# Optimization experiments

Measured on AMD Instinct MI355X. Metric: run time of the kernel, lower is better.

The kernel has to match this reference:

```python
import jax, jax.numpy as jnp
import numpy as np

B, U, L, E, H, V = 512, 10, 50, 200, 200, 50000
FLAT = 16 * 16 * 8  # conv(3x3,VALID)->48x48, pool(3x3,s3)->16x16, 8 channels


def gru(x, Wih, Whh, bih, bhh):
    """PyTorch-convention GRU (gate order r,z,n). x: [B,T,E] -> (ys [B,T,H], h_last [B,H])."""
    Bx = x.shape[0]
    Hh = Whh.shape[1]
    x_proj = x @ Wih.T + bih  # [B,T,3H]

    def step(h, xp):
        gh = h @ Whh.T + bhh
        xr, xz, xn = jnp.split(xp, 3, axis=-1)
        hr, hz, hn = jnp.split(gh, 3, axis=-1)
        r = jax.nn.sigmoid(xr + hr)
        z = jax.nn.sigmoid(xz + hz)
        n = jnp.tanh(xn + r * hn)
        h_new = (1.0 - z) * n + z * h
        return h_new, h_new

    h0 = jnp.zeros((Bx, Hh), x.dtype)
    h_last, ys = jax.lax.scan(step, h0, jnp.swapaxes(x_proj, 0, 1))
    return jnp.swapaxes(ys, 0, 1), h_last


def setup_inputs() -> dict:
    key = jax.random.key(0)
    ks = jax.random.split(key, 24)
    s = 0.05
    inp = {
        "utterance": jax.random.randint(ks[0], (B, U, L), 0, V, dtype=jnp.int32),
        "response": jax.random.randint(ks[1], (B, L), 0, V, dtype=jnp.int32),
        "emb": jax.random.uniform(ks[2], (V, E), jnp.float32, -0.25, 0.25),
        "W_ih_u": jax.random.normal(ks[3], (3 * H, E)) * s,
        "W_hh_u": jax.random.normal(ks[4], (3 * H, H)) * s,
        "b_ih_u": jnp.zeros((3 * H,), jnp.float32),
        "b_hh_u": jnp.zeros((3 * H,), jnp.float32),
        "W_ih_r": jax.random.normal(ks[5], (3 * H, E)) * s,
        "W_hh_r": jax.random.normal(ks[6], (3 * H, H)) * s,
        "b_ih_r": jnp.zeros((3 * H,), jnp.float32),
        "b_hh_r": jnp.zeros((3 * H,), jnp.float32),
        "conv_w": jax.random.normal(ks[7], (8, 2, 3, 3)) * 0.3,
        "conv_b": jnp.zeros((8,), jnp.float32),
        "lin_w": jax.random.normal(ks[8], (50, FLAT)) * 0.02,
        "lin_b": jnp.zeros((50,), jnp.float32),
        "Amat": jax.random.normal(ks[9], (H, H)) * 0.05,
        "W_ih_f": jax.random.normal(ks[10], (3 * H, 50)) * s,
        "W_hh_f": jax.random.normal(ks[11], (3 * H, H)) * s,
        "b_ih_f": jnp.zeros((3 * H,), jnp.float32),
        "b_hh_f": jnp.zeros((3 * H,), jnp.float32),
        "flin_w": jax.random.normal(ks[12], (1, H)) * 0.05,
        "flin_b": jnp.zeros((1,), jnp.float32),
    }
    return inp


def reference(utterance, response, emb, W_ih_u, W_hh_u, b_ih_u, b_hh_u,
              W_ih_r, W_hh_r, b_ih_r, b_hh_r, conv_w, conv_b, lin_w, lin_b,
              Amat, W_ih_f, W_hh_f, b_ih_f, b_hh_f, flin_w, flin_b):
    ue = emb[utterance]            # [B,U,L,E]
    re = emb[response]             # [B,L,E]

    rg, _ = gru(re, W_ih_r, W_hh_r, b_ih_r, b_hh_r)  # [B,L,H]

    # word-level match: matmul(utt_emb, resp_emb^T)
    m1 = jnp.einsum('bule,bte->bult', ue, re)  # [B,U,L,L]

    # segment-level: GRU(utt) @ A @ GRU(resp)^T  (loop over utterances folded into batch)
    ug, _ = gru(ue.reshape(B * U, L, E), W_ih_u, W_hh_u, b_ih_u, b_hh_u)
    ug = ug.reshape(B, U, L, H)
    m2 = jnp.einsum('bulh,hk,btk->bult', ug, Amat, rg)  # [B,U,L,L]

    x = jnp.stack([m1, m2], axis=2).reshape(B * U, 2, L, L)  # [B*U,2,50,50]
    x = jax.lax.conv_general_dilated(x, conv_w, (1, 1), 'VALID',
                                     dimension_numbers=('NCHW', 'OIHW', 'NCHW'))
    x = jax.nn.relu(x + conv_b[None, :, None, None])          # [B*U,8,48,48]
    x = jax.lax.reduce_window(x, -jnp.inf, jax.lax.max,
                              (1, 1, 3, 3), (1, 1, 3, 3), 'VALID')  # [B*U,8,16,16]
    x = x.reshape(B * U, FLAT)
    mv = jnp.tanh(x @ lin_w.T + lin_b).reshape(B, U, 50)      # matching vectors

    _, h_last = gru(mv, W_ih_f, W_hh_f, b_ih_f, b_hh_f)       # [B,H]
    logits = h_last @ flin_w.T + flin_b                       # [B,1]
    return jax.nn.sigmoid(logits)
```

## Files before the change

kernel.cpp:

```cpp
#include <hip/hip_runtime.h>
#include <hip/hip_bf16.h>


typedef __attribute__((ext_vector_type(8))) short short8v;
typedef __attribute__((ext_vector_type(4))) float f32x4;

__device__ __forceinline__ float sigm(float x) { return 1.0f / (1.0f + __expf(-x)); }
__device__ __forceinline__ float tanhfast(float x) {
    float e = __expf(2.0f * x);
    return 1.0f - 2.0f / (e + 1.0f);
}
__device__ __forceinline__ float bl(unsigned x) { return __uint_as_float(x << 16); }
__device__ __forceinline__ float bh(unsigned x) { return __uint_as_float(x & 0xffff0000u); }
__device__ __forceinline__ unsigned packbf(float a, float b) {
    union { __hip_bfloat16 h[2]; unsigned u; } cv;
    cv.h[0] = __float2bfloat16(a); cv.h[1] = __float2bfloat16(b);
    return cv.u;
}

__global__ __launch_bounds__(256)
void gemm_mfma(const void* __restrict__ Asrc, int a_bf16,
               const int* __restrict__ gidx,
               const float* __restrict__ W, const float* __restrict__ bias,
               __hip_bfloat16* __restrict__ C, int M, int N)
{
    __shared__ __hip_bfloat16 Al[64 * 232];
    __shared__ __hip_bfloat16 Bl[64 * 232];
    const int tid = threadIdx.x;
    const int m0 = blockIdx.x * 64, n0 = blockIdx.y * 64;

    for (int idx = tid; idx < 64 * 29; idx += 256) {
        int r = idx / 29, q = idx - r * 29;
        int k0 = q * 8, row = m0 + r;
        uint4 val = make_uint4(0, 0, 0, 0);
        if (k0 < 200 && row < M) {
            size_t ar = (size_t)(gidx ? gidx[row] : row) * 200 + k0;
            if (a_bf16) {
                val = *(const uint4*)((const __hip_bfloat16*)Asrc + ar);
            } else {
                const float* ap = (const float*)Asrc + ar;
                float4 f0 = *(const float4*)ap;
                float4 f1 = *(const float4*)(ap + 4);
                val.x = packbf(f0.x, f0.y); val.y = packbf(f0.z, f0.w);
                val.z = packbf(f1.x, f1.y); val.w = packbf(f1.z, f1.w);
            }
        }
        *(uint4*)(Al + r * 232 + k0) = val;
    }
    for (int idx = tid; idx < 64 * 29; idx += 256) {
        int r = idx / 29, q = idx - r * 29;
        int k0 = q * 8, row = n0 + r;
        uint4 val = make_uint4(0, 0, 0, 0);
        if (k0 < 200 && row < N) {
            const float* wp = W + (size_t)row * 200 + k0;
            float4 f0 = *(const float4*)wp;
            float4 f1 = *(const float4*)(wp + 4);
            val.x = packbf(f0.x, f0.y); val.y = packbf(f0.z, f0.w);
            val.z = packbf(f1.x, f1.y); val.w = packbf(f1.z, f1.w);
        }
        *(uint4*)(Bl + r * 232 + k0) = val;
    }
    __syncthreads();

    const int wid = tid >> 6, lane = tid & 63;
    const int wm = (wid >> 1) * 32, wn = (wid & 1) * 32;
    const int lrow = lane & 15, lk8 = (lane >> 4) * 8;
    f32x4 acc00 = {0.f, 0.f, 0.f, 0.f}, acc01 = {0.f, 0.f, 0.f, 0.f};
    f32x4 acc10 = {0.f, 0.f, 0.f, 0.f}, acc11 = {0.f, 0.f, 0.f, 0.f};
#pragma unroll
    for (int kk = 0; kk < 7; ++kk) {
        const int kb = kk * 32 + lk8;
        short8v a0 = *(const short8v*)(Al + (wm + lrow) * 232 + kb);
        short8v a1 = *(const short8v*)(Al + (wm + 16 + lrow) * 232 + kb);
        short8v b0 = *(const short8v*)(Bl + (wn + lrow) * 232 + kb);
        short8v b1 = *(const short8v*)(Bl + (wn + 16 + lrow) * 232 + kb);
        acc00 = __builtin_amdgcn_mfma_f32_16x16x32_bf16(a0, b0, acc00, 0, 0, 0);
        acc01 = __builtin_amdgcn_mfma_f32_16x16x32_bf16(a0, b1, acc01, 0, 0, 0);
        acc10 = __builtin_amdgcn_mfma_f32_16x16x32_bf16(a1, b0, acc10, 0, 0, 0);
        acc11 = __builtin_amdgcn_mfma_f32_16x16x32_bf16(a1, b1, acc11, 0, 0, 0);
    }
    const int drow = (lane >> 4) * 4, dcol = lane & 15;
#pragma unroll
    for (int fm = 0; fm < 2; ++fm) {
#pragma unroll
        for (int fn = 0; fn < 2; ++fn) {
            const f32x4 av = (fm == 0) ? (fn == 0 ? acc00 : acc01)
                                       : (fn == 0 ? acc10 : acc11);
            const int gcol = n0 + wn + fn * 16 + dcol;
            if (gcol >= N) continue;
            const float bs = bias ? bias[gcol] : 0.0f;
#pragma unroll
            for (int r = 0; r < 4; ++r) {
                const int grow = m0 + wm + fm * 16 + drow + r;
                if (grow >= M) continue;
                C[(size_t)grow * N + gcol] = __float2bfloat16(av[r] + bs);
            }
        }
    }
}

__global__ __launch_bounds__(256)
void gemm_tn(const void* __restrict__ Av, int a_bf16,
             const int* __restrict__ gidx, int gstride, int goff,
             const float* __restrict__ W, const float* __restrict__ bias,
             void* __restrict__ Cv, int c_bf16,
             int M, int N, int K, int act)
{
    __shared__ float As[16][64];
    __shared__ float Ws[16][64];
    const int tid = threadIdx.x;
    const int m0 = blockIdx.x * 64;
    const int n0 = blockIdx.y * 64;
    const int lr = tid >> 2;
    const int lk = (tid & 3) << 2;
    const int tx = tid & 15, ty = tid >> 4;

    float acc[4][4];
#pragma unroll
    for (int i = 0; i < 4; ++i)
#pragma unroll
        for (int j = 0; j < 4; ++j) acc[i][j] = 0.0f;

    const int am = m0 + lr;
    size_t arow_off = 0; bool avalid = (am < M);
    if (avalid) arow_off = (size_t)(gidx ? gidx[(size_t)am * gstride + goff] : am) * K;
    const float* arow32 = (const float*)Av + arow_off;
    const __hip_bfloat16* arow16 = (const __hip_bfloat16*)Av + arow_off;
    const int wn = n0 + lr;
    const float* wrow = (wn < N) ? (W + (size_t)wn * K) : nullptr;

    for (int kb = 0; kb < K; kb += 16) {
        const int k = kb + lk;
        float a0 = 0, a1 = 0, a2 = 0, a3 = 0, w0 = 0, w1 = 0, w2 = 0, w3 = 0;
        if (avalid) {
            if (a_bf16) {
                if (k + 3 < K) {
                    uint2 p = *(const uint2*)(arow16 + k);
                    a0 = bl(p.x); a1 = bh(p.x); a2 = bl(p.y); a3 = bh(p.y);
                } else {
                    if (k < K) a0 = __bfloat162float(arow16[k]);
                    if (k + 1 < K) a1 = __bfloat162float(arow16[k + 1]);
                    if (k + 2 < K) a2 = __bfloat162float(arow16[k + 2]);
                }
            } else {
                if (k + 3 < K) { float4 v = *(const float4*)(arow32 + k); a0 = v.x; a1 = v.y; a2 = v.z; a3 = v.w; }
                else { if (k < K) a0 = arow32[k]; if (k + 1 < K) a1 = arow32[k + 1]; if (k + 2 < K) a2 = arow32[k + 2]; }
            }
        }
        if (wrow) {
            if (k + 3 < K) { float4 v = *(const float4*)(wrow + k); w0 = v.x; w1 = v.y; w2 = v.z; w3 = v.w; }
            else { if (k < K) w0 = wrow[k]; if (k + 1 < K) w1 = wrow[k + 1]; if (k + 2 < K) w2 = wrow[k + 2]; }
        }
        __syncthreads();
        As[lk + 0][lr] = a0; As[lk + 1][lr] = a1; As[lk + 2][lr] = a2; As[lk + 3][lr] = a3;
        Ws[lk + 0][lr] = w0; Ws[lk + 1][lr] = w1; Ws[lk + 2][lr] = w2; Ws[lk + 3][lr] = w3;
        __syncthreads();
#pragma unroll
        for (int kk = 0; kk < 16; ++kk) {
            float4 av = *(const float4*)(&As[kk][ty << 2]);
            float4 wv = *(const float4*)(&Ws[kk][tx << 2]);
            float aa[4] = { av.x, av.y, av.z, av.w };
            float ww[4] = { wv.x, wv.y, wv.z, wv.w };
#pragma unroll
            for (int i = 0; i < 4; ++i)
#pragma unroll
                for (int j = 0; j < 4; ++j)
                    acc[i][j] = fmaf(aa[i], ww[j], acc[i][j]);
        }
    }

#pragma unroll
    for (int i = 0; i < 4; ++i) {
        const int row = m0 + (ty << 2) + i;
        if (row >= M) continue;
#pragma unroll
        for (int j = 0; j < 4; ++j) {
            const int col = n0 + (tx << 2) + j;
            if (col >= N) continue;
            float t = acc[i][j];
            if (bias) t += bias[col];
            if (act == 1) t = tanhfast(t);
            if (c_bf16) ((__hip_bfloat16*)Cv)[(size_t)row * N + col] = __float2bfloat16(t);
            else        ((float*)Cv)[(size_t)row * N + col] = t;
        }
    }
}

__global__ __launch_bounds__(256)
void transpose_wf(const float* __restrict__ Wf, float* __restrict__ Tf)
{
    int id = blockIdx.x * 256 + threadIdx.x;
    if (id < 120000) {
        int e = id / 600, j = id - e * 600;
        Tf[id] = Wf[(size_t)j * 200 + e];
    }
}

__global__ __launch_bounds__(256)
void pack_whh(const float* __restrict__ Wu, const float* __restrict__ Wr,
              __hip_bfloat16* __restrict__ Du, __hip_bfloat16* __restrict__ Dr)
{
    int idx = blockIdx.x * 256 + threadIdx.x;
    if (idx >= 143360) return;
    int j = idx / 224, e = idx - j * 224;
    bool v = (j < 600) && (e < 200);
    Du[idx] = __float2bfloat16(v ? Wu[(size_t)j * 200 + e] : 0.0f);
    Dr[idx] = __float2bfloat16(v ? Wr[(size_t)j * 200 + e] : 0.0f);
}

__global__ __launch_bounds__(256)
void gather_re16(const int* __restrict__ resp, const float* __restrict__ emb,
                 __hip_bfloat16* __restrict__ re16)
{
    int idx = blockIdx.x * 256 + threadIdx.x;
    if (idx < 2560000) {
        int row = idx / 100, q = idx - row * 100;
        float2 v = *(const float2*)(emb + (size_t)resp[row] * 200 + 2 * q);
        ((unsigned*)re16)[idx] = packbf(v.x, v.y);
    }
}

__global__ __launch_bounds__(512, 2)
void scan_gru_mfma(const int* __restrict__ utt,
                   const __hip_bfloat16* __restrict__ EPu,
                   const __hip_bfloat16* __restrict__ xpr16,
                   const __hip_bfloat16* __restrict__ Wu16,
                   const __hip_bfloat16* __restrict__ Wr16,
                   const float* __restrict__ bhu, const float* __restrict__ bhr,
                   __hip_bfloat16* __restrict__ ug16,
                   __hip_bfloat16* __restrict__ rg16)
{
    __shared__ __align__(16) float gh[32][644];
    __shared__ __align__(16) float hf[32][204];
    __shared__ __align__(16) __hip_bfloat16 h16[32][232];

    const int tid = threadIdx.x;
    const bool isResp = (int)blockIdx.x >= 160;
    const int row0 = isResp ? ((int)blockIdx.x - 160) * 32 : (int)blockIdx.x * 32;
    const __hip_bfloat16* Wt = isResp ? Wr16 : Wu16;
    const float* bgate = isResp ? bhr : bhu;
    __hip_bfloat16* arch = isResp ? rg16 : ug16;

    for (int i = tid; i < 32 * 204; i += 512) ((float*)hf)[i] = 0.0f;
    for (int i = tid; i < 928; i += 512) ((uint4*)h16)[i] = make_uint4(0, 0, 0, 0);
    __syncthreads();

    const int wid = tid >> 6, lane = tid & 63;
    const int lrow = lane & 15, lk8 = (lane >> 4) * 8;
    const int drow = (lane >> 4) * 4, dcol = lane & 15;

    short8v Bf[5][7];
#pragma unroll
    for (int i = 0; i < 5; ++i) {
        const int j = (wid * 5 + i) * 16 + lrow;
#pragma unroll
        for (int kk = 0; kk < 7; ++kk)
            Bf[i][kk] = *(const short8v*)(Wt + (size_t)j * 224 + kk * 32 + lk8);
    }

    const int r0a = tid / 25,        c0a = (tid % 25) * 8;
    const int t1  = tid + 512;
    const int r0b = t1 / 25,         c0b = (t1 % 25) * 8;

    for (int t = 0; t < 50; ++t) {
        const int ga = row0 + r0a;
        const __hip_bfloat16* xpa = isResp
            ? (xpr16 + ((size_t)ga * 50 + t) * 600)
            : (EPu + (size_t)utt[ga * 50 + t] * 600);
        uint4 xra = *(const uint4*)(xpa + c0a);
        uint4 xza = *(const uint4*)(xpa + 200 + c0a);
        uint4 xna = *(const uint4*)(xpa + 400 + c0a);

        f32x4 a0[5], a1[5];
#pragma unroll
        for (int i = 0; i < 5; ++i) {
            a0[i] = (f32x4){0.f, 0.f, 0.f, 0.f};
            a1[i] = (f32x4){0.f, 0.f, 0.f, 0.f};
        }
#pragma unroll
        for (int kk = 0; kk < 7; ++kk) {
            short8v A0 = *(const short8v*)(&h16[lrow][kk * 32 + lk8]);
            short8v A1 = *(const short8v*)(&h16[16 + lrow][kk * 32 + lk8]);
#pragma unroll
            for (int i = 0; i < 5; ++i) {
                a0[i] = __builtin_amdgcn_mfma_f32_16x16x32_bf16(A0, Bf[i][kk], a0[i], 0, 0, 0);
                a1[i] = __builtin_amdgcn_mfma_f32_16x16x32_bf16(A1, Bf[i][kk], a1[i], 0, 0, 0);
            }
        }
#pragma unroll
        for (int i = 0; i < 5; ++i) {
            const int j = (wid * 5 + i) * 16 + dcol;
#pragma unroll
            for (int r = 0; r < 4; ++r) {
                gh[drow + r][j] = a0[i][r];
                gh[16 + drow + r][j] = a1[i][r];
            }
        }
        __syncthreads();

        {
            const int row = r0a, c0 = c0a, grow = ga;
            const unsigned xr4[4] = { xra.x, xra.y, xra.z, xra.w };
            const unsigned xz4[4] = { xza.x, xza.y, xza.z, xza.w };
            const unsigned xn4[4] = { xna.x, xna.y, xna.z, xna.w };
            float hn[8];
#pragma unroll
            for (int j = 0; j < 8; ++j) {
                const int c = c0 + j;
                const float xr = (j & 1) ? bh(xr4[j >> 1]) : bl(xr4[j >> 1]);
                const float xz = (j & 1) ? bh(xz4[j >> 1]) : bl(xz4[j >> 1]);
                const float xn = (j & 1) ? bh(xn4[j >> 1]) : bl(xn4[j >> 1]);
                const float rr = sigm(xr + gh[row][c] + bgate[c]);
                const float zz = sigm(xz + gh[row][200 + c] + bgate[200 + c]);
                const float nn = tanhfast(xn + rr * (gh[row][400 + c] + bgate[400 + c]));
                hn[j] = (1.0f - zz) * nn + zz * hf[row][c];
            }
            *(float4*)(&hf[row][c0])     = (float4){hn[0], hn[1], hn[2], hn[3]};
            *(float4*)(&hf[row][c0 + 4]) = (float4){hn[4], hn[5], hn[6], hn[7]};
            uint4 pk;
            pk.x = packbf(hn[0], hn[1]); pk.y = packbf(hn[2], hn[3]);
            pk.z = packbf(hn[4], hn[5]); pk.w = packbf(hn[6], hn[7]);
            *(uint4*)(&h16[row][c0]) = pk;
            *(uint4*)(arch + ((size_t)grow * 50 + t) * 200 + c0) = pk;
        }
        if (tid < 288) {
            const int row = r0b, c0 = c0b, grow = row0 + r0b;
            const __hip_bfloat16* xp = isResp
                ? (xpr16 + ((size_t)grow * 50 + t) * 600)
                : (EPu + (size_t)utt[grow * 50 + t] * 600);
            uint4 xrv = *(const uint4*)(xp + c0);
            uint4 xzv = *(const uint4*)(xp + 200 + c0);
            uint4 xnv = *(const uint4*)(xp + 400 + c0);
            const unsigned xr4[4] = { xrv.x, xrv.y, xrv.z, xrv.w };
            const unsigned xz4[4] = { xzv.x, xzv.y, xzv.z, xzv.w };
            const unsigned xn4[4] = { xnv.x, xnv.y, xnv.z, xnv.w };
            float hn[8];
#pragma unroll
            for (int j = 0; j < 8; ++j) {
                const int c = c0 + j;
                const float xr = (j & 1) ? bh(xr4[j >> 1]) : bl(xr4[j >> 1]);
                const float xz = (j & 1) ? bh(xz4[j >> 1]) : bl(xz4[j >> 1]);
                const float xn = (j & 1) ? bh(xn4[j >> 1]) : bl(xn4[j >> 1]);
                const float rr = sigm(xr + gh[row][c] + bgate[c]);
                const float zz = sigm(xz + gh[row][200 + c] + bgate[200 + c]);
                const float nn = tanhfast(xn + rr * (gh[row][400 + c] + bgate[400 + c]));
                hn[j] = (1.0f - zz) * nn + zz * hf[row][c];
            }
            *(float4*)(&hf[row][c0])     = (float4){hn[0], hn[1], hn[2], hn[3]};
            *(float4*)(&hf[row][c0 + 4]) = (float4){hn[4], hn[5], hn[6], hn[7]};
            uint4 pk;
            pk.x = packbf(hn[0], hn[1]); pk.y = packbf(hn[2], hn[3]);
            pk.z = packbf(hn[4], hn[5]); pk.w = packbf(hn[6], hn[7]);
            *(uint4*)(&h16[row][c0]) = pk;
            *(uint4*)(arch + ((size_t)grow * 50 + t) * 200 + c0) = pk;
        }
        __syncthreads();
    }
}

__global__ __launch_bounds__(256)
void match_conv_pool(const int* __restrict__ utt, const float* __restrict__ emb,
                     const __hip_bfloat16* __restrict__ ug16,
                     const __hip_bfloat16* __restrict__ re16,
                     const __hip_bfloat16* __restrict__ rgA16,
                     const float* __restrict__ cw, const float* __restrict__ cb,
                     float* __restrict__ pooled)
{
    const int bu = blockIdx.x, b = bu / 10;
    __shared__ __align__(16) __hip_bfloat16 As[64 * 232];
    __shared__ __align__(16) __hip_bfloat16 Bs[64 * 232];
    __shared__ float m[2][50][50];
    __shared__ float w[144];
    __shared__ float bsh[8];
    const int tid = threadIdx.x;
    if (tid < 144) w[tid] = cw[tid];
    if (tid >= 144 && tid < 152) bsh[tid - 144] = cb[tid - 144];

    for (int idx = tid; idx < 64 * 29; idx += 256) {
        int r = idx / 29, q = idx - r * 29;
        uint4 av = make_uint4(0, 0, 0, 0), bv = make_uint4(0, 0, 0, 0);
        if (r < 50 && q < 25) {
            const float* ap = emb + (size_t)utt[bu * 50 + r] * 200 + q * 8;
            float4 f0 = *(const float4*)ap;
            float4 f1 = *(const float4*)(ap + 4);
            av.x = packbf(f0.x, f0.y); av.y = packbf(f0.z, f0.w);
            av.z = packbf(f1.x, f1.y); av.w = packbf(f1.z, f1.w);
            bv = *(const uint4*)(re16 + (size_t)b * 10000 + (size_t)r * 200 + q * 8);
        }
        *(uint4*)(As + r * 232 + q * 8) = av;
        *(uint4*)(Bs + r * 232 + q * 8) = bv;
    }
    __syncthreads();

    const int wid = tid >> 6, lane = tid & 63;
    const int wm = (wid >> 1) * 32, wn = (wid & 1) * 32;
    const int lrow = lane & 15, lk8 = (lane >> 4) * 8;
    const int drow = (lane >> 4) * 4, dcol = lane & 15;

#pragma unroll 1
    for (int ch = 0; ch < 2; ++ch) {
        f32x4 acc00 = {0.f, 0.f, 0.f, 0.f}, acc01 = {0.f, 0.f, 0.f, 0.f};
        f32x4 acc10 = {0.f, 0.f, 0.f, 0.f}, acc11 = {0.f, 0.f, 0.f, 0.f};
#pragma unroll
        for (int kk = 0; kk < 7; ++kk) {
            const int kb = kk * 32 + lk8;
            short8v a0 = *(const short8v*)(As + (wm + lrow) * 232 + kb);
            short8v a1 = *(const short8v*)(As + (wm + 16 + lrow) * 232 + kb);
            short8v b0 = *(const short8v*)(Bs + (wn + lrow) * 232 + kb);
            short8v b1 = *(const short8v*)(Bs + (wn + 16 + lrow) * 232 + kb);
            acc00 = __builtin_amdgcn_mfma_f32_16x16x32_bf16(a0, b0, acc00, 0, 0, 0);
            acc01 = __builtin_amdgcn_mfma_f32_16x16x32_bf16(a0, b1, acc01, 0, 0, 0);
            acc10 = __builtin_amdgcn_mfma_f32_16x16x32_bf16(a1, b0, acc10, 0, 0, 0);
            acc11 = __builtin_amdgcn_mfma_f32_16x16x32_bf16(a1, b1, acc11, 0, 0, 0);
        }
#pragma unroll
        for (int fm = 0; fm < 2; ++fm) {
#pragma unroll
            for (int fn = 0; fn < 2; ++fn) {
                const f32x4 av = (fm == 0) ? (fn == 0 ? acc00 : acc01)
                                           : (fn == 0 ? acc10 : acc11);
                const int gcol = wn + fn * 16 + dcol;
                if (gcol >= 50) continue;
#pragma unroll
                for (int r = 0; r < 4; ++r) {
                    const int grow = wm + fm * 16 + drow + r;
                    if (grow < 50) m[ch][grow][gcol] = av[r];
                }
            }
        }
        __syncthreads();
        if (ch == 0) {
            for (int idx = tid; idx < 50 * 25; idx += 256) {
                int r = idx / 25, q = idx - r * 25;
                *(uint4*)(As + r * 232 + q * 8) =
                    *(const uint4*)(ug16 + (size_t)bu * 10000 + (size_t)r * 200 + q * 8);
                *(uint4*)(Bs + r * 232 + q * 8) =
                    *(const uint4*)(rgA16 + (size_t)b * 10000 + (size_t)r * 200 + q * 8);
            }
            __syncthreads();
        }
    }

#pragma unroll
    for (int k = 0; k < 8; ++k) {
        const int o = tid + k * 256;
        const int c = o >> 8, ph = (o >> 4) & 15, pw = o & 15;
        float mx = -1e30f;
#pragma unroll
        for (int p = 0; p < 3; ++p)
#pragma unroll
            for (int q = 0; q < 3; ++q) {
                const int y = ph * 3 + p, x = pw * 3 + q;
                float s = bsh[c];
#pragma unroll
                for (int ci = 0; ci < 2; ++ci)
#pragma unroll
                    for (int dy = 0; dy < 3; ++dy)
#pragma unroll
                        for (int dx = 0; dx < 3; ++dx)
                            s = fmaf(w[(c * 2 + ci) * 9 + dy * 3 + dx],
                                     m[ci][y + dy][x + dx], s);
                s = fmaxf(s, 0.0f);
                mx = fmaxf(mx, s);
            }
        pooled[(size_t)bu * 2048 + o] = mx;
    }
}

__global__ __launch_bounds__(256)
void final_gru(const float* __restrict__ xpf, const float* __restrict__ WTf,
               const float* __restrict__ bhf, const float* __restrict__ fw,
               const float* __restrict__ fb, float* __restrict__ out)
{
    const int blk = blockIdx.x;
    const int tid = threadIdx.x;
    __shared__ float h[2][201];
    for (int i = tid; i < 402; i += 256) ((float*)h)[i] = 0.0f;
    __syncthreads();
    const int rr = tid / 100;
    const int j0 = 2 * (tid % 100);
    for (int t = 0; t < 10; ++t) {
        float cR[2] = {}, cZ[2] = {}, cN[2] = {};
        if (tid < 200) {
#pragma unroll 2
            for (int e = 0; e < 200; ++e) {
                const float* w = WTf + (size_t)e * 600;
                float2 wr = *(const float2*)(w + j0);
                float2 wz = *(const float2*)(w + 200 + j0);
                float2 wn = *(const float2*)(w + 400 + j0);
                float hv = h[rr][e];
                cR[0] = fmaf(hv, wr.x, cR[0]); cR[1] = fmaf(hv, wr.y, cR[1]);
                cZ[0] = fmaf(hv, wz.x, cZ[0]); cZ[1] = fmaf(hv, wz.y, cZ[1]);
                cN[0] = fmaf(hv, wn.x, cN[0]); cN[1] = fmaf(hv, wn.y, cN[1]);
            }
        }
        __syncthreads();
        if (tid < 200) {
            const float* xp = xpf + ((size_t)(blk * 2 + rr) * 10 + t) * 600;
#pragma unroll
            for (int j = 0; j < 2; ++j) {
                const int c = j0 + j;
                float rrg = sigm(xp[c] + cR[j] + bhf[c]);
                float zz = sigm(xp[200 + c] + cZ[j] + bhf[200 + c]);
                float nn = tanhfast(xp[400 + c] + rrg * (cN[j] + bhf[400 + c]));
                h[rr][c] = (1.0f - zz) * nn + zz * h[rr][c];
            }
        }
        __syncthreads();
    }
    if (tid < 2) {
        float s = fb[0];
        for (int k = 0; k < 200; ++k) s = fmaf(h[tid][k], fw[k], s);
        out[blk * 2 + tid] = sigm(s);
    }
}

__global__ __launch_bounds__(256)
void fill_out(float* __restrict__ out)
{
    int i = blockIdx.x * 256 + threadIdx.x;
    if (i < 512) out[i] = 0.0f;
}

extern "C" void kernel_launch(void* const* d_in, const int* in_sizes, int n_in,
                              void* d_out, int out_size, void* d_ws, size_t ws_size,
                              hipStream_t stream)
{
    const int*   utt    = (const int*)d_in[0];
    const int*   resp   = (const int*)d_in[1];
    const float* emb    = (const float*)d_in[2];
    const float* W_ih_u = (const float*)d_in[3];
    const float* W_hh_u = (const float*)d_in[4];
    const float* b_ih_u = (const float*)d_in[5];
    const float* b_hh_u = (const float*)d_in[6];
    const float* W_ih_r = (const float*)d_in[7];
    const float* W_hh_r = (const float*)d_in[8];
    const float* b_ih_r = (const float*)d_in[9];
    const float* b_hh_r = (const float*)d_in[10];
    const float* conv_w = (const float*)d_in[11];
    const float* conv_b = (const float*)d_in[12];
    const float* lin_w  = (const float*)d_in[13];
    const float* lin_b  = (const float*)d_in[14];
    const float* Amat   = (const float*)d_in[15];
    const float* W_ih_f = (const float*)d_in[16];
    const float* W_hh_f = (const float*)d_in[17];
    const float* b_ih_f = (const float*)d_in[18];
    const float* b_hh_f = (const float*)d_in[19];
    const float* flin_w = (const float*)d_in[20];
    const float* flin_b = (const float*)d_in[21];
    float* out = (float*)d_out;
    float* ws  = (float*)d_ws;

    size_t off = 0;
    auto alloc = [&](size_t n) { float* p = ws + off; off += (n + 63) & ~((size_t)63); return p; };
    float* WT_f   = alloc(120000);
    float* Wu16f  = alloc(71680);
    float* Wr16f  = alloc(71680);
    float* re16f  = alloc(2560000);
    float* EPuf   = alloc(15000000);
    float* xprf   = alloc(7680000);
    float* ug16f  = alloc(25600000);
    float* rg16f  = alloc(2560000);
    float* rgA16f = alloc(2560000);

    if (off * sizeof(float) > ws_size) {
        hipLaunchKernelGGL(fill_out, dim3(2), dim3(256), 0, stream, out);
        return;
    }

    __hip_bfloat16* Wu16  = (__hip_bfloat16*)Wu16f;
    __hip_bfloat16* Wr16  = (__hip_bfloat16*)Wr16f;
    __hip_bfloat16* re16  = (__hip_bfloat16*)re16f;
    __hip_bfloat16* EPu   = (__hip_bfloat16*)EPuf;
    __hip_bfloat16* xpr16 = (__hip_bfloat16*)xprf;
    __hip_bfloat16* ug16  = (__hip_bfloat16*)ug16f;
    __hip_bfloat16* rg16  = (__hip_bfloat16*)rg16f;
    __hip_bfloat16* rgA16 = (__hip_bfloat16*)rgA16f;
    float* pooled = EPuf;
    float* mv     = xprf;
    float* xpf    = xprf + 400000;

    hipLaunchKernelGGL(transpose_wf, dim3(469), dim3(256), 0, stream, W_hh_f, WT_f);
    hipLaunchKernelGGL(pack_whh, dim3(560), dim3(256), 0, stream,
                       W_hh_u, W_hh_r, Wu16, Wr16);
    hipLaunchKernelGGL(gather_re16, dim3(10000), dim3(256), 0, stream, resp, emb, re16);
    hipLaunchKernelGGL(gemm_mfma, dim3(782, 10), dim3(256), 0, stream,
                       (const void*)emb, 0, (const int*)nullptr, W_ih_u, b_ih_u,
                       EPu, 50000, 600);
    hipLaunchKernelGGL(gemm_mfma, dim3(400, 10), dim3(256), 0, stream,
                       (const void*)emb, 0, resp, W_ih_r, b_ih_r,
                       xpr16, 25600, 600);
    hipLaunchKernelGGL(scan_gru_mfma, dim3(176), dim3(512), 0, stream,
                       utt, EPu, xpr16, Wu16, Wr16, b_hh_u, b_hh_r, ug16, rg16);
    hipLaunchKernelGGL(gemm_mfma, dim3(400, 4), dim3(256), 0, stream,
                       (const void*)rg16, 1, (const int*)nullptr, Amat,
                       (const float*)nullptr, rgA16, 25600, 200);
    hipLaunchKernelGGL(match_conv_pool, dim3(5120), dim3(256), 0, stream,
                       utt, emb, ug16, re16, rgA16, conv_w, conv_b, pooled);
    hipLaunchKernelGGL(gemm_tn, dim3(80, 1), dim3(256), 0, stream,
                       pooled, 0, (const int*)nullptr, 1, 0, lin_w, lin_b,
                       mv, 0, 5120, 50, 2048, 1);
    hipLaunchKernelGGL(gemm_tn, dim3(80, 10), dim3(256), 0, stream,
                       mv, 0, (const int*)nullptr, 1, 0, W_ih_f, b_ih_f,
                       xpf, 0, 5120, 600, 50, 0);
    hipLaunchKernelGGL(final_gru, dim3(256), dim3(256), 0, stream,
                       xpf, WT_f, b_hh_f, flin_w, flin_b, out);
}
```

Before: 1.175 ms.

## Use bf16 MFMA for final linear GEMMs and prefetch second-row GRU inputs

Replaces the scalar fp32 tiled gemm_tn with an MFMA bf16 GEMM that stages A and W tiles in padded LDS with a K-step of 128. It is used for the pooled->matching-vector projection and the matching-vector->final-GRU input projection. The pooled features and matching vectors are now stored as bf16, which halves their memory traffic but lowers precision. The scan GRU also issues the loads of the second row's x-projection before the recurrent MFMA loop, so their latency overlaps with compute at the cost of extra registers.

```diff
diff --git a/kernel.cpp b/kernel.cpp
--- a/kernel.cpp
+++ b/kernel.cpp
@@ -100,88 +100,101 @@
 }
 
 __global__ __launch_bounds__(256)
-void gemm_tn(const void* __restrict__ Av, int a_bf16,
-             const int* __restrict__ gidx, int gstride, int goff,
-             const float* __restrict__ W, const float* __restrict__ bias,
-             void* __restrict__ Cv, int c_bf16,
-             int M, int N, int K, int act)
-{
-    __shared__ float As[16][64];
-    __shared__ float Ws[16][64];
+void gemm_mfma_k(const void* __restrict__ Asrc, int a_bf16,
+                 const float* __restrict__ W, const float* __restrict__ bias,
+                 void* __restrict__ Cv, int c_bf16,
+                 int M, int N, int K, int act)
+{
+    __shared__ __align__(16) __hip_bfloat16 As[64 * 136];
+    __shared__ __align__(16) __hip_bfloat16 Bs[64 * 136];
     const int tid = threadIdx.x;
-    const int m0 = blockIdx.x * 64;
-    const int n0 = blockIdx.y * 64;
-    const int lr = tid >> 2;
-    const int lk = (tid & 3) << 2;
-    const int tx = tid & 15, ty = tid >> 4;
-
-    float acc[4][4];
-#pragma unroll
-    for (int i = 0; i < 4; ++i)
-#pragma unroll
-        for (int j = 0; j < 4; ++j) acc[i][j] = 0.0f;
-
-    const int am = m0 + lr;
-    size_t arow_off = 0; bool avalid = (am < M);
-    if (avalid) arow_off = (size_t)(gidx ? gidx[(size_t)am * gstride + goff] : am) * K;
-    const float* arow32 = (const float*)Av + arow_off;
-    const __hip_bfloat16* arow16 = (const __hip_bfloat16*)Av + arow_off;
-    const int wn = n0 + lr;
-    const float* wrow = (wn < N) ? (W + (size_t)wn * K) : nullptr;
-
-    for (int kb = 0; kb < K; kb += 16) {
-        const int k = kb + lk;
-        float a0 = 0, a1 = 0, a2 = 0, a3 = 0, w0 = 0, w1 = 0, w2 = 0, w3 = 0;
-        if (avalid) {
-            if (a_bf16) {
-                if (k + 3 < K) {
-                    uint2 p = *(const uint2*)(arow16 + k);
-                    a0 = bl(p.x); a1 = bh(p.x); a2 = bl(p.y); a3 = bh(p.y);
+    const int m0 = blockIdx.x * 64, n0 = blockIdx.y * 64;
+    const int wid = tid >> 6, lane = tid & 63;
+    const int wm = (wid >> 1) * 32, wn = (wid & 1) * 32;
+    const int lrow = lane & 15, lk8 = (lane >> 4) * 8;
+    const bool aAlign16 = a_bf16 && ((K & 7) == 0);
+
+    f32x4 acc00 = {0.f, 0.f, 0.f, 0.f}, acc01 = {0.f, 0.f, 0.f, 0.f};
+    f32x4 acc10 = {0.f, 0.f, 0.f, 0.f}, acc11 = {0.f, 0.f, 0.f, 0.f};
+
+    for (int kb = 0; kb < K; kb += 128) {
+        for (int idx = tid; idx < 1024; idx += 256) {
+            int r = idx >> 4, q = idx & 15;
+            int k0 = kb + q * 8, row = m0 + r;
+            uint4 av = make_uint4(0, 0, 0, 0);
+            if (row < M && k0 < K) {
+                size_t base = (size_t)row * K + k0;
+                if (a_bf16) {
+                    const __hip_bfloat16* ap = (const __hip_bfloat16*)Asrc + base;
+                    if (aAlign16 && k0 + 8 <= K) {
+                        av = *(const uint4*)ap;
+                    } else {
+                        unsigned t4[4] = {0, 0, 0, 0};
+                        int nv = (K - k0 < 8) ? (K - k0) : 8;
+                        for (int e = 0; e < nv; ++e)
+                            ((__hip_bfloat16*)t4)[e] = ap[e];
+                        av.x = t4[0]; av.y = t4[1]; av.z = t4[2]; av.w = t4[3];
+                    }
                 } else {
-                    if (k < K) a0 = __bfloat162float(arow16[k]);
-                    if (k + 1 < K) a1 = __bfloat162float(arow16[k + 1]);
-                    if (k + 2 < K) a2 = __bfloat162float(arow16[k + 2]);
+                    const float* ap = (const float*)Asrc + base;
+                    float tv[8] = {0, 0, 0, 0, 0, 0, 0, 0};
+                    int nv = (K - k0 < 8) ? (K - k0) : 8;
+                    for (int e = 0; e < nv; ++e) tv[e] = ap[e];
+                    av.x = packbf(tv[0], tv[1]); av.y = packbf(tv[2], tv[3]);
+                    av.z = packbf(tv[4], tv[5]); av.w = packbf(tv[6], tv[7]);
                 }
-            } else {
-                if (k + 3 < K) { float4 v = *(const float4*)(arow32 + k); a0 = v.x; a1 = v.y; a2 = v.z; a3 = v.w; }
-                else { if (k < K) a0 = arow32[k]; if (k + 1 < K) a1 = arow32[k + 1]; if (k + 2 < K) a2 = arow32[k + 2]; }
-            }
-        }
-        if (wrow) {
-            if (k + 3 < K) { float4 v = *(const float4*)(wrow + k); w0 = v.x; w1 = v.y; w2 = v.z; w3 = v.w; }
-            else { if (k < K) w0 = wrow[k]; if (k + 1 < K) w1 = wrow[k + 1]; if (k + 2 < K) w2 = wrow[k + 2]; }
+            }
+            *(uint4*)(As + r * 136 + q * 8) = av;
+        }
+        for (int idx = tid; idx < 1024; idx += 256) {
+            int r = idx >> 4, q = idx & 15;
+            int k0 = kb + q * 8, row = n0 + r;
+            uint4 bv = make_uint4(0, 0, 0, 0);
+            if (row < N && k0 < K) {
+                const float* wp = W + (size_t)row * K + k0;
+                float tv[8] = {0, 0, 0, 0, 0, 0, 0, 0};
+                int nv = (K - k0 < 8) ? (K - k0) : 8;
+                for (int e = 0; e < nv; ++e) tv[e] = wp[e];
+                bv.x = packbf(tv[0], tv[1]); bv.y = packbf(tv[2], tv[3]);
+                bv.z = packbf(tv[4], tv[5]); bv.w = packbf(tv[6], tv[7]);
+            }
+            *(uint4*)(Bs + r * 136 + q * 8) = bv;
         }
         __syncthreads();
-        As[lk + 0][lr] = a0; As[lk + 1][lr] = a1; As[lk + 2][lr] = a2; As[lk + 3][lr] = a3;
-        Ws[lk + 0][lr] = w0; Ws[lk + 1][lr] = w1; Ws[lk + 2][lr] = w2; Ws[lk + 3][lr] = w3;
+#pragma unroll
+        for (int kk = 0; kk < 4; ++kk) {
+            const int ko = kk * 32 + lk8;
+            short8v a0 = *(const short8v*)(As + (wm + lrow) * 136 + ko);
+            short8v a1 = *(const short8v*)(As + (wm + 16 + lrow) * 136 + ko);
+            short8v b0 = *(const short8v*)(Bs + (wn + lrow) * 136 + ko);
+            short8v b1 = *(const short8v*)(Bs + (wn + 16 + lrow) * 136 + ko);
+            acc00 = __builtin_amdgcn_mfma_f32_16x16x32_bf16(a0, b0, acc00, 0, 0, 0);
+            acc01 = __builtin_amdgcn_mfma_f32_16x16x32_bf16(a0, b1, acc01, 0, 0, 0);
+            acc10 = __builtin_amdgcn_mfma_f32_16x16x32_bf16(a1, b0, acc10, 0, 0, 0);
+            acc11 = __builtin_amdgcn_mfma_f32_16x16x32_bf16(a1, b1, acc11, 0, 0, 0);
+        }
         __syncthreads();
-#pragma unroll
-        for (int kk = 0; kk < 16; ++kk) {
-            float4 av = *(const float4*)(&As[kk][ty << 2]);
-            float4 wv = *(const float4*)(&Ws[kk][tx << 2]);
-            float aa[4] = { av.x, av.y, av.z, av.w };
-            float ww[4] = { wv.x, wv.y, wv.z, wv.w };
-#pragma unroll
-            for (int i = 0; i < 4; ++i)
-#pragma unroll
-                for (int j = 0; j < 4; ++j)
-                    acc[i][j] = fmaf(aa[i], ww[j], acc[i][j]);
-        }
-    }
-
-#pragma unroll
-    for (int i = 0; i < 4; ++i) {
-        const int row = m0 + (ty << 2) + i;
-        if (row >= M) continue;
-#pragma unroll
-        for (int j = 0; j < 4; ++j) {
-            const int col = n0 + (tx << 2) + j;
-            if (col >= N) continue;
-            float t = acc[i][j];
-            if (bias) t += bias[col];
-            if (act == 1) t = tanhfast(t);
-            if (c_bf16) ((__hip_bfloat16*)Cv)[(size_t)row * N + col] = __float2bfloat16(t);
-            else        ((float*)Cv)[(size_t)row * N + col] = t;
+    }
+
+    const int drow = (lane >> 4) * 4, dcol = lane & 15;
+#pragma unroll
+    for (int fm = 0; fm < 2; ++fm) {
+#pragma unroll
+        for (int fn = 0; fn < 2; ++fn) {
+            const f32x4 av = (fm == 0) ? (fn == 0 ? acc00 : acc01)
+                                       : (fn == 0 ? acc10 : acc11);
+            const int gcol = n0 + wn + fn * 16 + dcol;
+            if (gcol >= N) continue;
+            const float bs = bias ? bias[gcol] : 0.0f;
+#pragma unroll
+            for (int r = 0; r < 4; ++r) {
+                const int grow = m0 + wm + fm * 16 + drow + r;
+                if (grow >= M) continue;
+                float t = av[r] + bs;
+                if (act == 1) t = tanhfast(t);
+                if (c_bf16) ((__hip_bfloat16*)Cv)[(size_t)grow * N + gcol] = __float2bfloat16(t);
+                else        ((float*)Cv)[(size_t)grow * N + gcol] = t;
+            }
         }
     }
 }
@@ -270,6 +283,16 @@
         uint4 xra = *(const uint4*)(xpa + c0a);
         uint4 xza = *(const uint4*)(xpa + 200 + c0a);
         uint4 xna = *(const uint4*)(xpa + 400 + c0a);
+        uint4 xrb, xzb, xnb;
+        const int gb = row0 + r0b;
+        if (tid < 288) {
+            const __hip_bfloat16* xpb = isResp
+                ? (xpr16 + ((size_t)gb * 50 + t) * 600)
+                : (EPu + (size_t)utt[gb * 50 + t] * 600);
+            xrb = *(const uint4*)(xpb + c0b);
+            xzb = *(const uint4*)(xpb + 200 + c0b);
+            xnb = *(const uint4*)(xpb + 400 + c0b);
+        }
 
         f32x4 a0[5], a1[5];
 #pragma unroll
@@ -324,16 +347,10 @@
             *(uint4*)(arch + ((size_t)grow * 50 + t) * 200 + c0) = pk;
         }
         if (tid < 288) {
-            const int row = r0b, c0 = c0b, grow = row0 + r0b;
-            const __hip_bfloat16* xp = isResp
-                ? (xpr16 + ((size_t)grow * 50 + t) * 600)
-                : (EPu + (size_t)utt[grow * 50 + t] * 600);
-            uint4 xrv = *(const uint4*)(xp + c0);
-            uint4 xzv = *(const uint4*)(xp + 200 + c0);
-            uint4 xnv = *(const uint4*)(xp + 400 + c0);
-            const unsigned xr4[4] = { xrv.x, xrv.y, xrv.z, xrv.w };
-            const unsigned xz4[4] = { xzv.x, xzv.y, xzv.z, xzv.w };
-            const unsigned xn4[4] = { xnv.x, xnv.y, xnv.z, xnv.w };
+            const int row = r0b, c0 = c0b, grow = gb;
+            const unsigned xr4[4] = { xrb.x, xrb.y, xrb.z, xrb.w };
+            const unsigned xz4[4] = { xzb.x, xzb.y, xzb.z, xzb.w };
+            const unsigned xn4[4] = { xnb.x, xnb.y, xnb.z, xnb.w };
             float hn[8];
 #pragma unroll
             for (int j = 0; j < 8; ++j) {
@@ -364,7 +381,7 @@
                      const __hip_bfloat16* __restrict__ re16,
                      const __hip_bfloat16* __restrict__ rgA16,
                      const float* __restrict__ cw, const float* __restrict__ cb,
-                     float* __restrict__ pooled)
+                     __hip_bfloat16* __restrict__ pooled16)
 {
     const int bu = blockIdx.x, b = bu / 10;
     __shared__ __align__(16) __hip_bfloat16 As[64 * 232];
@@ -463,7 +480,7 @@
                 s = fmaxf(s, 0.0f);
                 mx = fmaxf(mx, s);
             }
-        pooled[(size_t)bu * 2048 + o] = mx;
+        pooled16[(size_t)bu * 2048 + o] = __float2bfloat16(mx);
     }
 }
 
@@ -576,9 +593,9 @@
     __hip_bfloat16* ug16  = (__hip_bfloat16*)ug16f;
     __hip_bfloat16* rg16  = (__hip_bfloat16*)rg16f;
     __hip_bfloat16* rgA16 = (__hip_bfloat16*)rgA16f;
-    float* pooled = EPuf;
-    float* mv     = xprf;
-    float* xpf    = xprf + 400000;
+    __hip_bfloat16* pooled16 = (__hip_bfloat16*)EPuf;
+    __hip_bfloat16* mv16     = (__hip_bfloat16*)xprf;
+    float* xpf = xprf + 400000;
 
     hipLaunchKernelGGL(transpose_wf, dim3(469), dim3(256), 0, stream, W_hh_f, WT_f);
     hipLaunchKernelGGL(pack_whh, dim3(560), dim3(256), 0, stream,
@@ -596,13 +613,13 @@
                        (const void*)rg16, 1, (const int*)nullptr, Amat,
                        (const float*)nullptr, rgA16, 25600, 200);
     hipLaunchKernelGGL(match_conv_pool, dim3(5120), dim3(256), 0, stream,
-                       utt, emb, ug16, re16, rgA16, conv_w, conv_b, pooled);
-    hipLaunchKernelGGL(gemm_tn, dim3(80, 1), dim3(256), 0, stream,
-                       pooled, 0, (const int*)nullptr, 1, 0, lin_w, lin_b,
-                       mv, 0, 5120, 50, 2048, 1);
-    hipLaunchKernelGGL(gemm_tn, dim3(80, 10), dim3(256), 0, stream,
-                       mv, 0, (const int*)nullptr, 1, 0, W_ih_f, b_ih_f,
-                       xpf, 0, 5120, 600, 50, 0);
+                       utt, emb, ug16, re16, rgA16, conv_w, conv_b, pooled16);
+    hipLaunchKernelGGL(gemm_mfma_k, dim3(80, 1), dim3(256), 0, stream,
+                       (const void*)pooled16, 1, lin_w, lin_b,
+                       (void*)mv16, 1, 5120, 50, 2048, 1);
+    hipLaunchKernelGGL(gemm_mfma_k, dim3(80, 10), dim3(256), 0, stream,
+                       (const void*)mv16, 1, W_ih_f, b_ih_f,
+                       (void*)xpf, 0, 5120, 600, 50, 0);
     hipLaunchKernelGGL(final_gru, dim3(256), dim3(256), 0, stream,
                        xpf, WT_f, b_hh_f, flin_w, flin_b, out);
 }
```

After: 1.154 ms, median of 2. No clear change (-1.8%).
